# Performance work log

Measured on AMD Instinct MI355X. Metric: run time of the kernel, lower is better.

The kernel has to match this reference:

```python
import jax, jax.numpy as jnp
import numpy as np

IN, OUT, ST = 64, 64, 256
D = IN + OUT + ST  # 384, concat(x, prev_output, state)
NET1 = [D, 1024, 1024, OUT]
NET3 = [D] + NET1 + [ST]  # [384,384,1024,1024,64,256]
NW = sum(NET3[i] * NET3[i + 1] for i in range(len(NET3) - 1))  # 1671168
NB = sum(NET3[1:])  # 2752
NET2 = [D] + NET1 + [NW + NB]  # last layer: 64 -> 1673920


def setup_inputs() -> dict:
    key = jax.random.key(0)
    ks = iter(jax.random.split(key, 64))
    d = {"x": jax.random.normal(next(ks), (IN,), jnp.float32)}
    for i in range(len(NET1) - 1):
        d[f"w1_{i}"] = jax.random.normal(next(ks), (NET1[i + 1], NET1[i]), jnp.float32) / np.sqrt(NET1[i])
        d[f"b1_{i}"] = jnp.zeros((NET1[i + 1],), jnp.float32)
    for i in range(len(NET2) - 1):
        d[f"w2_{i}"] = jax.random.normal(next(ks), (NET2[i + 1], NET2[i]), jnp.float32) / np.sqrt(NET2[i])
        d[f"b2_{i}"] = jnp.zeros((NET2[i + 1],), jnp.float32)
    for i in range(len(NET3) - 1):
        d[f"w3_{i}"] = jax.random.normal(next(ks), (NET3[i + 1], NET3[i]), jnp.float32) * 0.02
        d[f"b3_{i}"] = jnp.zeros((NET3[i + 1],), jnp.float32)
    d["prev_output"] = jnp.zeros((OUT,), jnp.float32)
    d["state"] = jnp.zeros((ST,), jnp.float32)
    d["prev_weight_change"] = jax.random.normal(next(ks), (NW,), jnp.float32) * 0.01
    d["prev_bias_change"] = jax.random.normal(next(ks), (NB,), jnp.float32) * 0.01
    return d


def _mlp(x, layers):
    for w, b in layers:
        x = jax.nn.relu(x @ w.T + b)
    return x


def reference(x, w1_0, b1_0, w1_1, b1_1, w1_2, b1_2,
              w2_0, b2_0, w2_1, b2_1, w2_2, b2_2, w2_3, b2_3, w2_4, b2_4,
              w3_0, b3_0, w3_1, b3_1, w3_2, b3_2, w3_3, b3_3, w3_4, b3_4,
              prev_output, state, prev_weight_change, prev_bias_change):
    inpt = jnp.concatenate([x, prev_output, state])  # [D]
    # net2: hypernetwork producing next step's fast-weight deltas
    x2 = _mlp(inpt, [(w2_0, b2_0), (w2_1, b2_1), (w2_2, b2_2), (w2_3, b2_3), (w2_4, b2_4)])
    weight_change = x2[:NW]
    bias_change = x2[NW:]
    # update net3 fast weights with PREVIOUS step's deltas (as in the torch code)
    w3 = [w3_0, w3_1, w3_2, w3_3, w3_4]
    b3 = [b3_0, b3_1, b3_2, b3_3, b3_4]
    new_w, off = [], 0
    for w in w3:
        n = w.shape[0] * w.shape[1]
        new_w.append(w + prev_weight_change[off:off + n].reshape(w.shape))
        off += n
    new_b, off = [], 0
    for b in b3:
        n = b.shape[0]
        new_b.append(b + prev_bias_change[off:off + n])
        off += n
    # net3: state update with fast weights
    x3 = _mlp(inpt, list(zip(new_w, new_b)))  # new state (side-effect in torch)
    # net1: output head
    x1 = _mlp(inpt, [(w1_0, b1_0), (w1_1, b1_1), (w1_2, b1_2)])
    # weight_change/bias_change/x3 become next-step state in the torch module;
    # the forward return value is x1 only.
    del weight_change, bias_change, x3
    return x1
```

## Files before the change

### kernel.cpp

```cpp
#include <hip/hip_runtime.h>


__device__ __forceinline__ float wave_reduce_sum(float v) {
    v += __shfl_xor(v, 32, 64);
    v += __shfl_xor(v, 16, 64);
    v += __shfl_xor(v, 8, 64);
    v += __shfl_xor(v, 4, 64);
    v += __shfl_xor(v, 2, 64);
    v += __shfl_xor(v, 1, 64);
    return v;
}

__global__ void __launch_bounds__(256) fc_relu_concat(
        const float* __restrict__ x, const float* __restrict__ po,
        const float* __restrict__ st,
        const float* __restrict__ w, const float* __restrict__ b,
        float* __restrict__ out) {
    __shared__ float s_in[384];
    const int t = threadIdx.x;
    for (int i = t; i < 384; i += 256) {
        float v;
        if (i < 64)       v = x[i];
        else if (i < 128) v = po[i - 64];
        else              v = st[i - 128];
        s_in[i] = v;
    }
    __syncthreads();

    const int wave = t >> 6;
    const int lane = t & 63;
    const int r = blockIdx.x * 4 + wave;

    const float* wr = w + (size_t)r * 384;
    float acc = 0.f;
    {
        const int idx = lane * 4;
        float4 wv = *reinterpret_cast<const float4*>(wr + idx);
        float4 iv = *reinterpret_cast<const float4*>(s_in + idx);
        acc += wv.x * iv.x + wv.y * iv.y + wv.z * iv.z + wv.w * iv.w;
    }
    {
        const int idx = 256 + lane * 2;
        float2 wv = *reinterpret_cast<const float2*>(wr + idx);
        float2 iv = *reinterpret_cast<const float2*>(s_in + idx);
        acc += wv.x * iv.x + wv.y * iv.y;
    }
    acc = wave_reduce_sum(acc);
    if (lane == 0) out[r] = fmaxf(acc + b[r], 0.f);
}

__global__ void __launch_bounds__(256) fc_relu_1024(
        const float* __restrict__ w, const float* __restrict__ b,
        const float* __restrict__ in, float* __restrict__ out, int rows) {
    __shared__ float s_in[1024];
    const int t = threadIdx.x;
    for (int i = t; i < 1024; i += 256) s_in[i] = in[i];
    __syncthreads();

    const int wave = t >> 6;
    const int lane = t & 63;
    const int r = blockIdx.x * 4 + wave;
    if (r >= rows) return;

    const float* wr = w + (size_t)r * 1024;
    float acc = 0.f;
#pragma unroll
    for (int it = 0; it < 4; ++it) {
        const int idx = it * 256 + lane * 4;
        float4 wv = *reinterpret_cast<const float4*>(wr + idx);
        float4 iv = *reinterpret_cast<const float4*>(s_in + idx);
        acc += wv.x * iv.x + wv.y * iv.y + wv.z * iv.z + wv.w * iv.w;
    }
    acc = wave_reduce_sum(acc);
    if (lane == 0) out[r] = fmaxf(acc + b[r], 0.f);
}

extern "C" void kernel_launch(void* const* d_in, const int* in_sizes, int n_in,
                              void* d_out, int out_size, void* d_ws, size_t ws_size,
                              hipStream_t stream) {
    const float* x    = (const float*)d_in[0];
    const float* w1_0 = (const float*)d_in[1];
    const float* b1_0 = (const float*)d_in[2];
    const float* w1_1 = (const float*)d_in[3];
    const float* b1_1 = (const float*)d_in[4];
    const float* w1_2 = (const float*)d_in[5];
    const float* b1_2 = (const float*)d_in[6];
    const float* po   = (const float*)d_in[27];
    const float* st   = (const float*)d_in[28];

    float* out = (float*)d_out;
    float* h1 = (float*)d_ws;
    float* h2 = h1 + 1024;

    fc_relu_concat<<<256, 256, 0, stream>>>(x, po, st, w1_0, b1_0, h1);
    fc_relu_1024<<<256, 256, 0, stream>>>(w1_1, b1_1, h1, h2, 1024);
    fc_relu_1024<<<16, 256, 0, stream>>>(w1_2, b1_2, h2, out, 64);
}
```

Measured before the change: 15.72 us.

## Fuse three MLP layers into one persistent kernel with grid barriers

Replaces the three per-layer kernel launches with one kernel of 256 blocks. The blocks synchronise between layers through an atomic-counter grid barrier in workspace, which is zeroed each call with a memset. This removes two launch gaps and the idle time between dependent kernels. In exchange it relies on all 256 blocks being resident at once, adds spin-wait barrier latency, and adds a memset launch.

```diff
diff --git a/kernel.cpp b/kernel.cpp
--- a/kernel.cpp
+++ b/kernel.cpp
@@ -1,5 +1,7 @@
 #include <hip/hip_runtime.h>
 
+
+#define GRID 256
 
 __device__ __forceinline__ float wave_reduce_sum(float v) {
     v += __shfl_xor(v, 32, 64);
@@ -11,13 +13,45 @@
     return v;
 }
 
-__global__ void __launch_bounds__(256) fc_relu_concat(
+__device__ __forceinline__ unsigned long long bar_arrive(unsigned long long* ctr) {
+    __syncthreads();
+    unsigned long long old = 0;
+    if (threadIdx.x == 0) {
+        __threadfence();
+        old = __hip_atomic_fetch_add(ctr, 1ULL, __ATOMIC_ACQ_REL,
+                                     __HIP_MEMORY_SCOPE_AGENT);
+    }
+    return old;
+}
+
+__device__ __forceinline__ void bar_wait(unsigned long long* ctr,
+                                         unsigned long long old) {
+    if (threadIdx.x == 0) {
+        unsigned long long target = (old / GRID + 1) * (unsigned long long)GRID;
+        while (__hip_atomic_load(ctr, __ATOMIC_ACQUIRE,
+                                 __HIP_MEMORY_SCOPE_AGENT) < target) {
+            __builtin_amdgcn_s_sleep(1);
+        }
+        __threadfence();
+    }
+    __syncthreads();
+}
+
+__global__ void __launch_bounds__(256, 2) smrnn_fused(
         const float* __restrict__ x, const float* __restrict__ po,
         const float* __restrict__ st,
-        const float* __restrict__ w, const float* __restrict__ b,
-        float* __restrict__ out) {
-    __shared__ float s_in[384];
+        const float* __restrict__ w0, const float* __restrict__ b0,
+        const float* __restrict__ w1, const float* __restrict__ b1,
+        const float* __restrict__ w2, const float* __restrict__ b2,
+        float* __restrict__ h1, float* __restrict__ h2,
+        float* __restrict__ out, unsigned long long* __restrict__ ctr) {
+    __shared__ float s_in[1024];
     const int t = threadIdx.x;
+    const int lane = t & 63;
+    const int wave = t >> 6;
+    const int blk = blockIdx.x;
+    const int r = blk * 4 + wave;
+
     for (int i = t; i < 384; i += 256) {
         float v;
         if (i < 64)       v = x[i];
@@ -27,52 +61,65 @@
     }
     __syncthreads();
 
-    const int wave = t >> 6;
-    const int lane = t & 63;
-    const int r = blockIdx.x * 4 + wave;
+    {
+        const float* wr = w0 + (size_t)r * 384;
+        float acc = 0.f;
+        {
+            const int idx = lane * 4;
+            float4 wv = *reinterpret_cast<const float4*>(wr + idx);
+            float4 iv = *reinterpret_cast<const float4*>(s_in + idx);
+            acc += wv.x * iv.x + wv.y * iv.y + wv.z * iv.z + wv.w * iv.w;
+        }
+        {
+            const int idx = 256 + lane * 2;
+            float2 wv = *reinterpret_cast<const float2*>(wr + idx);
+            float2 iv = *reinterpret_cast<const float2*>(s_in + idx);
+            acc += wv.x * iv.x + wv.y * iv.y;
+        }
+        acc = wave_reduce_sum(acc);
+        if (lane == 0) h1[r] = fmaxf(acc + b0[r], 0.f);
+    }
 
-    const float* wr = w + (size_t)r * 384;
-    float acc = 0.f;
-    {
-        const int idx = lane * 4;
-        float4 wv = *reinterpret_cast<const float4*>(wr + idx);
-        float4 iv = *reinterpret_cast<const float4*>(s_in + idx);
-        acc += wv.x * iv.x + wv.y * iv.y + wv.z * iv.z + wv.w * iv.w;
-    }
-    {
-        const int idx = 256 + lane * 2;
-        float2 wv = *reinterpret_cast<const float2*>(wr + idx);
-        float2 iv = *reinterpret_cast<const float2*>(s_in + idx);
-        acc += wv.x * iv.x + wv.y * iv.y;
-    }
-    acc = wave_reduce_sum(acc);
-    if (lane == 0) out[r] = fmaxf(acc + b[r], 0.f);
-}
+    bar_wait(ctr, bar_arrive(ctr));
 
-__global__ void __launch_bounds__(256) fc_relu_1024(
-        const float* __restrict__ w, const float* __restrict__ b,
-        const float* __restrict__ in, float* __restrict__ out, int rows) {
-    __shared__ float s_in[1024];
-    const int t = threadIdx.x;
-    for (int i = t; i < 1024; i += 256) s_in[i] = in[i];
+    for (int i = t; i < 1024; i += 256) s_in[i] = h1[i];
     __syncthreads();
 
-    const int wave = t >> 6;
-    const int lane = t & 63;
-    const int r = blockIdx.x * 4 + wave;
-    if (r >= rows) return;
+    {
+        const float* wr = w1 + (size_t)r * 1024;
+        float acc = 0.f;
+#pragma unroll
+        for (int it = 0; it < 4; ++it) {
+            const int idx = it * 256 + lane * 4;
+            float4 wv = *reinterpret_cast<const float4*>(wr + idx);
+            float4 iv = *reinterpret_cast<const float4*>(s_in + idx);
+            acc += wv.x * iv.x + wv.y * iv.y + wv.z * iv.z + wv.w * iv.w;
+        }
+        acc = wave_reduce_sum(acc);
+        if (lane == 0) h2[r] = fmaxf(acc + b1[r], 0.f);
+    }
 
-    const float* wr = w + (size_t)r * 1024;
-    float acc = 0.f;
+    unsigned long long old = bar_arrive(ctr);
+    if (blk >= 16) return;
+    bar_wait(ctr, old);
+
+    for (int i = t; i < 1024; i += 256) s_in[i] = h2[i];
+    __syncthreads();
+
+    {
+        const int r3 = blk * 4 + wave;
+        const float* wr = w2 + (size_t)r3 * 1024;
+        float acc = 0.f;
 #pragma unroll
-    for (int it = 0; it < 4; ++it) {
-        const int idx = it * 256 + lane * 4;
-        float4 wv = *reinterpret_cast<const float4*>(wr + idx);
-        float4 iv = *reinterpret_cast<const float4*>(s_in + idx);
-        acc += wv.x * iv.x + wv.y * iv.y + wv.z * iv.z + wv.w * iv.w;
+        for (int it = 0; it < 4; ++it) {
+            const int idx = it * 256 + lane * 4;
+            float4 wv = *reinterpret_cast<const float4*>(wr + idx);
+            float4 iv = *reinterpret_cast<const float4*>(s_in + idx);
+            acc += wv.x * iv.x + wv.y * iv.y + wv.z * iv.z + wv.w * iv.w;
+        }
+        acc = wave_reduce_sum(acc);
+        if (lane == 0) out[r3] = fmaxf(acc + b2[r3], 0.f);
     }
-    acc = wave_reduce_sum(acc);
-    if (lane == 0) out[r] = fmaxf(acc + b[r], 0.f);
 }
 
 extern "C" void kernel_launch(void* const* d_in, const int* in_sizes, int n_in,
@@ -89,10 +136,12 @@
     const float* st   = (const float*)d_in[28];
 
     float* out = (float*)d_out;
-    float* h1 = (float*)d_ws;
+    unsigned long long* ctr = (unsigned long long*)d_ws;
+    float* h1 = (float*)d_ws + 64;
     float* h2 = h1 + 1024;
 
-    fc_relu_concat<<<256, 256, 0, stream>>>(x, po, st, w1_0, b1_0, h1);
-    fc_relu_1024<<<256, 256, 0, stream>>>(w1_1, b1_1, h1, h2, 1024);
-    fc_relu_1024<<<16, 256, 0, stream>>>(w1_2, b1_2, h2, out, 64);
+    hipMemsetAsync(d_ws, 0, 64, stream);
+    smrnn_fused<<<GRID, 256, 0, stream>>>(x, po, st,
+                                          w1_0, b1_0, w1_1, b1_1, w1_2, b1_2,
+                                          h1, h2, out, ctr);
 }
```

Result: slower. 39.02 us (+148.2%).

## Fuse layers 2 and 3 via split-K atomics and last-block finalize

Applied to the files above, without the earlier changes.

Merges the second and third linear layers into one kernel. Each block computes four hidden units, contributes their partial products to the 64 outputs with atomicAdd, and the last block to finish (found with a global counter) applies bias and ReLU. The first kernel now zeroes the output and resets the counter. This removes one kernel launch and the h2 round trip, at the cost of 64x256 float atomics and a non-deterministic summation order.

```diff
diff --git a/kernel.cpp b/kernel.cpp
--- a/kernel.cpp
+++ b/kernel.cpp
@@ -1,5 +1,7 @@
 #include <hip/hip_runtime.h>
 
+
+#define GRID2 256
 
 __device__ __forceinline__ float wave_reduce_sum(float v) {
     v += __shfl_xor(v, 32, 64);
@@ -11,13 +13,20 @@
     return v;
 }
 
-__global__ void __launch_bounds__(256) fc_relu_concat(
+__global__ void __launch_bounds__(256) k1_layer1(
         const float* __restrict__ x, const float* __restrict__ po,
         const float* __restrict__ st,
-        const float* __restrict__ w, const float* __restrict__ b,
-        float* __restrict__ out) {
+        const float* __restrict__ w0, const float* __restrict__ b0,
+        float* __restrict__ h1, float* __restrict__ out,
+        unsigned int* __restrict__ ctr) {
     __shared__ float s_in[384];
     const int t = threadIdx.x;
+
+    if (blockIdx.x == 0) {
+        if (t < 64) out[t] = 0.f;
+        if (t == 0) *ctr = 0u;
+    }
+
     for (int i = t; i < 384; i += 256) {
         float v;
         if (i < 64)       v = x[i];
@@ -27,11 +36,11 @@
     }
     __syncthreads();
 
+    const int lane = t & 63;
     const int wave = t >> 6;
-    const int lane = t & 63;
     const int r = blockIdx.x * 4 + wave;
 
-    const float* wr = w + (size_t)r * 384;
+    const float* wr = w0 + (size_t)r * 384;
     float acc = 0.f;
     {
         const int idx = lane * 4;
@@ -46,33 +55,64 @@
         acc += wv.x * iv.x + wv.y * iv.y;
     }
     acc = wave_reduce_sum(acc);
-    if (lane == 0) out[r] = fmaxf(acc + b[r], 0.f);
+    if (lane == 0) h1[r] = fmaxf(acc + b0[r], 0.f);
 }
 
-__global__ void __launch_bounds__(256) fc_relu_1024(
-        const float* __restrict__ w, const float* __restrict__ b,
-        const float* __restrict__ in, float* __restrict__ out, int rows) {
+__global__ void __launch_bounds__(256) k2_layer23(
+        const float* __restrict__ w1, const float* __restrict__ b1,
+        const float* __restrict__ w2, const float* __restrict__ b2,
+        const float* __restrict__ h1, float* __restrict__ out,
+        unsigned int* __restrict__ ctr) {
     __shared__ float s_in[1024];
+    __shared__ float s_h2[4];
+    __shared__ unsigned int s_old;
+
     const int t = threadIdx.x;
-    for (int i = t; i < 1024; i += 256) s_in[i] = in[i];
+    const int lane = t & 63;
+    const int wave = t >> 6;
+    const int blk = blockIdx.x;
+
+    {
+        float4 v = *reinterpret_cast<const float4*>(h1 + t * 4);
+        *reinterpret_cast<float4*>(s_in + t * 4) = v;
+    }
     __syncthreads();
 
-    const int wave = t >> 6;
-    const int lane = t & 63;
-    const int r = blockIdx.x * 4 + wave;
-    if (r >= rows) return;
+    {
+        const int r = blk * 4 + wave;
+        const float* wr = w1 + (size_t)r * 1024;
+        float acc = 0.f;
+#pragma unroll
+        for (int it = 0; it < 4; ++it) {
+            const int idx = it * 256 + lane * 4;
+            float4 wv = *reinterpret_cast<const float4*>(wr + idx);
+            float4 iv = *reinterpret_cast<const float4*>(s_in + idx);
+            acc += wv.x * iv.x + wv.y * iv.y + wv.z * iv.z + wv.w * iv.w;
+        }
+        acc = wave_reduce_sum(acc);
+        if (lane == 0) s_h2[wave] = fmaxf(acc + b1[r], 0.f);
+    }
+    __syncthreads();
 
-    const float* wr = w + (size_t)r * 1024;
-    float acc = 0.f;
-#pragma unroll
-    for (int it = 0; it < 4; ++it) {
-        const int idx = it * 256 + lane * 4;
-        float4 wv = *reinterpret_cast<const float4*>(wr + idx);
-        float4 iv = *reinterpret_cast<const float4*>(s_in + idx);
-        acc += wv.x * iv.x + wv.y * iv.y + wv.z * iv.z + wv.w * iv.w;
+    if (wave == 0) {
+        const float* w2r = w2 + (size_t)lane * 1024 + blk * 4;
+        float4 wv = *reinterpret_cast<const float4*>(w2r);
+        float p = wv.x * s_h2[0] + wv.y * s_h2[1] + wv.z * s_h2[2] + wv.w * s_h2[3];
+        atomicAdd(out + lane, p);
     }
-    acc = wave_reduce_sum(acc);
-    if (lane == 0) out[r] = fmaxf(acc + b[r], 0.f);
+    __syncthreads();
+
+    if (t == 0) {
+        s_old = __hip_atomic_fetch_add(ctr, 1u, __ATOMIC_ACQ_REL,
+                                       __HIP_MEMORY_SCOPE_AGENT);
+    }
+    __syncthreads();
+
+    if (s_old == GRID2 - 1 && wave == 0) {
+        float pre = __hip_atomic_load(out + lane, __ATOMIC_ACQUIRE,
+                                      __HIP_MEMORY_SCOPE_AGENT);
+        out[lane] = fmaxf(pre + b2[lane], 0.f);
+    }
 }
 
 extern "C" void kernel_launch(void* const* d_in, const int* in_sizes, int n_in,
@@ -89,10 +129,9 @@
     const float* st   = (const float*)d_in[28];
 
     float* out = (float*)d_out;
-    float* h1 = (float*)d_ws;
-    float* h2 = h1 + 1024;
+    unsigned int* ctr = (unsigned int*)d_ws;
+    float* h1 = (float*)d_ws + 64;
 
-    fc_relu_concat<<<256, 256, 0, stream>>>(x, po, st, w1_0, b1_0, h1);
-    fc_relu_1024<<<256, 256, 0, stream>>>(w1_1, b1_1, h1, h2, 1024);
-    fc_relu_1024<<<16, 256, 0, stream>>>(w1_2, b1_2, h2, out, 64);
+    k1_layer1<<<256, 256, 0, stream>>>(x, po, st, w1_0, b1_0, h1, out, ctr);
+    k2_layer23<<<GRID2, 256, 0, stream>>>(w1_1, b1_1, w1_2, b1_2, h1, out, ctr);
 }
```

After: 19.09 us. 21.4% more time.
